# Kernel optimization log

Measured on AMD Instinct MI355X. Metric: run time of the kernel, lower is better.

The kernel has to match this reference:

```python
import jax, jax.numpy as jnp
import numpy as np

EPS = 1e-8            # EpisodicMemory.eps
TEMPERATURE = 0.25    # default temperature in query()


def setup_inputs() -> dict:
    key = jax.random.key(0)
    k1, k2, k3 = jax.random.split(key, 3)
    B, N, KD, VD, TOPK = 512, 500000, 128, 64, 16
    queries = jax.random.normal(k1, (B, KD), dtype=jnp.float32)
    # stored keys are L2-normalized at insert time
    keys = jax.random.normal(k2, (N, KD), dtype=jnp.float32)
    keys = keys / jnp.clip(jnp.linalg.norm(keys, axis=1, keepdims=True), EPS, None)
    values = jax.random.normal(k3, (N, VD), dtype=jnp.float32)
    return {"queries": queries, "keys": keys, "values": values, "topk": TOPK}


def reference(queries, keys, values, topk):
    # cosine similarity: normalize queries (keys already normalized in memory)
    qn = queries / jnp.clip(jnp.linalg.norm(queries, axis=1, keepdims=True), EPS, None)
    scores = (qn @ keys.T) / max(1e-6, TEMPERATURE)          # [B, N]
    topv, topidx = jax.lax.top_k(scores, topk)               # [B, K], [B, K]
    # stable exp-softmax with eps in the denominator (as in torch source)
    topv_exp = jnp.exp(topv - jnp.max(topv, axis=1, keepdims=True))
    topw = topv_exp / (jnp.sum(topv_exp, axis=1, keepdims=True) + EPS)
    vals = values[topidx]                                    # gather: [B, K, VD]
    retrieved = jnp.einsum('bk,bkd->bd', topw, vals)         # [B, VD]
    return retrieved, topw, topidx
```

## Files before the change

### kernel.cpp

```cpp
#include <hip/hip_runtime.h>
#include <hip/hip_bf16.h>

#define NB 512
#define KD 128
#define VD 64
#define NKEYS 500000
#define TOPK 16
#define CH 1024
#define NCHUNK 489
#define NCAND (NCHUNK*4)

typedef __attribute__((ext_vector_type(8))) short bf8s;
typedef __attribute__((ext_vector_type(4))) float f4;

__device__ __forceinline__ unsigned f2bf(float x) {
  union { float f; unsigned u; } v; v.f = x;
  return (v.u + 0x7fffu + ((v.u >> 16) & 1u)) >> 16;
}

__global__ __launch_bounds__(128) void qnorm_kernel(const float* __restrict__ q,
                                                    float* __restrict__ qn_f,
                                                    short* __restrict__ qn_bf) {
  int b = blockIdx.x, t = threadIdx.x;
  float x = q[b*KD + t];
  float s = x * x;
  #pragma unroll
  for (int o = 32; o > 0; o >>= 1) s += __shfl_down(s, o);
  __shared__ float p[2];
  if ((t & 63) == 0) p[t >> 6] = s;
  __syncthreads();
  float norm = sqrtf(p[0] + p[1]);
  norm = fmaxf(norm, 1e-8f);
  float v = x * (4.0f / norm);
  qn_f[b*KD + t] = v;
  qn_bf[b*KD + t] = (short)f2bf(v);
}

__global__ __launch_bounds__(256) void score_filter_kernel(
    const float* __restrict__ keys, const short* __restrict__ qn_bf,
    float* __restrict__ cand_val, int* __restrict__ cand_idx) {
  __shared__ float slds[256 * 17];
  const int chunk = blockIdx.x, gy = blockIdx.y;
  const int tid  = threadIdx.x;
  const int wave = tid >> 6, lane = tid & 63;
  const int col  = lane & 15, quad = lane >> 4;

  bf8s afrag[4][4];
  const int qbase = gy*256 + wave*64;
  #pragma unroll
  for (int mt = 0; mt < 4; mt++)
    #pragma unroll
    for (int ks = 0; ks < 4; ks++)
      afrag[mt][ks] = *(const bf8s*)(qn_bf + (qbase + mt*16 + col)*KD + ks*32 + quad*8);

  float tv0=-1e30f, tv1=-1e30f, tv2=-1e30f, tv3=-1e30f;
  int   ti0=0, ti1=0, ti2=0, ti3=0;
  const int nchunk0 = chunk * CH;

  for (int nt = 0; nt < CH/16; nt++) {
    const int nb = nchunk0 + nt*16;
    int r = nb + col; if (r > NKEYS-1) r = NKEYS-1;
    const float* kp = keys + (size_t)r*KD + quad*8;
    bf8s bfrag[4];
    #pragma unroll
    for (int ks = 0; ks < 4; ks++) {
      f4 x0 = *(const f4*)(kp + ks*32);
      f4 x1 = *(const f4*)(kp + ks*32 + 4);
      bf8s tt;
      tt[0]=(short)f2bf(x0[0]); tt[1]=(short)f2bf(x0[1]);
      tt[2]=(short)f2bf(x0[2]); tt[3]=(short)f2bf(x0[3]);
      tt[4]=(short)f2bf(x1[0]); tt[5]=(short)f2bf(x1[1]);
      tt[6]=(short)f2bf(x1[2]); tt[7]=(short)f2bf(x1[3]);
      bfrag[ks] = tt;
    }
    f4 acc[4];
    #pragma unroll
    for (int mt = 0; mt < 4; mt++) { acc[mt][0]=0.f; acc[mt][1]=0.f; acc[mt][2]=0.f; acc[mt][3]=0.f; }
    #pragma unroll
    for (int ks = 0; ks < 4; ks++)
      #pragma unroll
      for (int mt = 0; mt < 4; mt++)
        acc[mt] = __builtin_amdgcn_mfma_f32_16x16x32_bf16(afrag[mt][ks], bfrag[ks], acc[mt], 0, 0, 0);
    #pragma unroll
    for (int mt = 0; mt < 4; mt++)
      #pragma unroll
      for (int rg = 0; rg < 4; rg++)
        slds[(wave*64 + mt*16 + quad*4 + rg)*17 + col] = acc[mt][rg];
    __syncthreads();
    #pragma unroll
    for (int c = 0; c < 16; c++) {
      int n = nb + c;
      float v = slds[tid*17 + c];
      if (v > tv3 && n < NKEYS) {
        if (v > tv0)      { tv3=tv2;ti3=ti2; tv2=tv1;ti2=ti1; tv1=tv0;ti1=ti0; tv0=v;ti0=n; }
        else if (v > tv1) { tv3=tv2;ti3=ti2; tv2=tv1;ti2=ti1; tv1=v;ti1=n; }
        else if (v > tv2) { tv3=tv2;ti3=ti2; tv2=v;ti2=n; }
        else              { tv3=v;ti3=n; }
      }
    }
    __syncthreads();
  }
  const int gq = gy*256 + tid;
  const size_t o = ((size_t)gq*NCHUNK + chunk)*4;
  cand_val[o+0]=tv0; cand_val[o+1]=tv1; cand_val[o+2]=tv2; cand_val[o+3]=tv3;
  cand_idx[o+0]=ti0; cand_idx[o+1]=ti1; cand_idx[o+2]=ti2; cand_idx[o+3]=ti3;
}

__global__ __launch_bounds__(256) void merge_rescore_kernel(
    const float* __restrict__ qn_f, const float* __restrict__ keys,
    const float* __restrict__ values, const float* __restrict__ cand_val,
    const int* __restrict__ cand_idx, float* __restrict__ out) {
  const int b = blockIdx.x, t = threadIdx.x;
  const int lane = t & 63, wave = t >> 6;
  __shared__ float cv[NCAND]; __shared__ int ci[NCAND];
  __shared__ float qs[KD];
  __shared__ float redv[4]; __shared__ int redp[4];
  __shared__ float rv[32];  __shared__ int ri[32];
  __shared__ float sval[16]; __shared__ int sidx[16]; __shared__ float sw[16];

  if (t < KD) qs[t] = qn_f[b*KD + t];
  for (int i = t; i < NCAND; i += 256) {
    cv[i] = cand_val[(size_t)b*NCAND + i];
    ci[i] = cand_idx[(size_t)b*NCAND + i];
  }
  __syncthreads();

  for (int rdx = 0; rdx < 32; rdx++) {
    float mv = -1e30f; int mp = 0;
    for (int i = t; i < NCAND; i += 256) { float v = cv[i]; if (v > mv) { mv = v; mp = i; } }
    #pragma unroll
    for (int o = 32; o > 0; o >>= 1) {
      float ov = __shfl_down(mv, o); int op = __shfl_down(mp, o);
      if (ov > mv) { mv = ov; mp = op; }
    }
    if (lane == 0) { redv[wave] = mv; redp[wave] = mp; }
    __syncthreads();
    if (t == 0) {
      float bv = redv[0]; int bp = redp[0];
      for (int w = 1; w < 4; w++) if (redv[w] > bv) { bv = redv[w]; bp = redp[w]; }
      ri[rdx] = ci[bp];
      cv[bp] = -1e30f;
    }
    __syncthreads();
  }

  {
    int c = t >> 3, dg = t & 7;
    int n = ri[c];
    const float* kr = keys + (size_t)n*KD + dg*16;
    float part = 0.f;
    #pragma unroll
    for (int j = 0; j < 16; j++) part += kr[j] * qs[dg*16 + j];
    #pragma unroll
    for (int o = 4; o > 0; o >>= 1) part += __shfl_down(part, o, 8);
    if (dg == 0) rv[c] = part;
  }
  __syncthreads();

  if (t < 32) {
    float v = rv[t]; int idx = ri[t];
    int rank = 0;
    for (int j = 0; j < 32; j++) {
      float vj = rv[j]; int ij = ri[j];
      rank += (vj > v) || (vj == v && ij < idx);
    }
    if (rank < TOPK) { sval[rank] = v; sidx[rank] = idx; }
  }
  __syncthreads();

  if (t < TOPK) {
    float m = sval[0];
    float e = expf(sval[t] - m);
    float s = e;
    #pragma unroll
    for (int o = 8; o > 0; o >>= 1) s += __shfl_down(s, o, 16);
    s = __shfl(s, 0, 16);
    float w = e / (s + 1e-8f);
    sw[t] = w;
    out[NB*VD + b*TOPK + t] = w;
    out[NB*VD + NB*TOPK + b*TOPK + t] = (float)sidx[t];
  }
  __syncthreads();

  if (t < VD) {
    float acc = 0.f;
    #pragma unroll
    for (int k = 0; k < TOPK; k++) acc += sw[k] * values[(size_t)sidx[k]*VD + t];
    out[b*VD + t] = acc;
  }
}

extern "C" void kernel_launch(void* const* d_in, const int* in_sizes, int n_in,
                              void* d_out, int out_size, void* d_ws, size_t ws_size,
                              hipStream_t stream) {
  const float* queries = (const float*)d_in[0];
  const float* keys    = (const float*)d_in[1];
  const float* values  = (const float*)d_in[2];
  float* out = (float*)d_out;

  char* ws = (char*)d_ws;
  float* qn_f  = (float*)ws;
  short* qn_bf = (short*)(ws + (size_t)NB*KD*4);
  float* cand_val = (float*)(ws + (size_t)NB*KD*4 + (size_t)NB*KD*2);
  int*   cand_idx = (int*)((char*)cand_val + (size_t)NB*NCHUNK*4*sizeof(float));

  qnorm_kernel<<<NB, KD, 0, stream>>>(queries, qn_f, qn_bf);
  score_filter_kernel<<<dim3(NCHUNK, 2), 256, 0, stream>>>(keys, qn_bf, cand_val, cand_idx);
  merge_rescore_kernel<<<NB, 256, 0, stream>>>(qn_f, keys, values, cand_val, cand_idx, out);
}
```

Baseline: 659.2 us.

## Radix-select candidate merge and prefetch key rows in score kernel

The merge kernel replaces 32 rounds of block-wide argmax over ~2000 candidates with a radix histogram select on the float bits. The select keeps up to 64 survivors at or above the threshold and rescores them in fp32 before ranking to top-16. The score kernel software-prefetches the next 16 key rows into registers during current compute and uses raw barriers that wait only on LDS. This cuts the serial barrier-heavy selection and hides global load latency, at the cost of more registers and a larger rescoring set.

```diff
diff --git a/kernel.cpp b/kernel.cpp
--- a/kernel.cpp
+++ b/kernel.cpp
@@ -9,6 +9,7 @@
 #define CH 1024
 #define NCHUNK 489
 #define NCAND (NCHUNK*4)
+#define CBUF 64
 
 typedef __attribute__((ext_vector_type(8))) short bf8s;
 typedef __attribute__((ext_vector_type(4))) float f4;
@@ -16,6 +17,11 @@
 __device__ __forceinline__ unsigned f2bf(float x) {
   union { float f; unsigned u; } v; v.f = x;
   return (v.u + 0x7fffu + ((v.u >> 16) & 1u)) >> 16;
+}
+
+__device__ __forceinline__ void barrier_lgkm() {
+  asm volatile("s_waitcnt lgkmcnt(0)" ::: "memory");
+  __builtin_amdgcn_s_barrier();
 }
 
 __global__ __launch_bounds__(128) void qnorm_kernel(const float* __restrict__ q,
@@ -57,21 +63,37 @@
   int   ti0=0, ti1=0, ti2=0, ti3=0;
   const int nchunk0 = chunk * CH;
 
+  f4 x0[4], x1[4];
+  {
+    int r = nchunk0 + col; if (r > NKEYS-1) r = NKEYS-1;
+    const float* kp = keys + (size_t)r*KD + quad*8;
+    #pragma unroll
+    for (int ks = 0; ks < 4; ks++) {
+      x0[ks] = *(const f4*)(kp + ks*32);
+      x1[ks] = *(const f4*)(kp + ks*32 + 4);
+    }
+  }
+
   for (int nt = 0; nt < CH/16; nt++) {
     const int nb = nchunk0 + nt*16;
-    int r = nb + col; if (r > NKEYS-1) r = NKEYS-1;
-    const float* kp = keys + (size_t)r*KD + quad*8;
     bf8s bfrag[4];
     #pragma unroll
     for (int ks = 0; ks < 4; ks++) {
-      f4 x0 = *(const f4*)(kp + ks*32);
-      f4 x1 = *(const f4*)(kp + ks*32 + 4);
       bf8s tt;
-      tt[0]=(short)f2bf(x0[0]); tt[1]=(short)f2bf(x0[1]);
-      tt[2]=(short)f2bf(x0[2]); tt[3]=(short)f2bf(x0[3]);
-      tt[4]=(short)f2bf(x1[0]); tt[5]=(short)f2bf(x1[1]);
-      tt[6]=(short)f2bf(x1[2]); tt[7]=(short)f2bf(x1[3]);
+      tt[0]=(short)f2bf(x0[ks][0]); tt[1]=(short)f2bf(x0[ks][1]);
+      tt[2]=(short)f2bf(x0[ks][2]); tt[3]=(short)f2bf(x0[ks][3]);
+      tt[4]=(short)f2bf(x1[ks][0]); tt[5]=(short)f2bf(x1[ks][1]);
+      tt[6]=(short)f2bf(x1[ks][2]); tt[7]=(short)f2bf(x1[ks][3]);
       bfrag[ks] = tt;
+    }
+    if (nt + 1 < CH/16) {
+      int r = nb + 16 + col; if (r > NKEYS-1) r = NKEYS-1;
+      const float* kp = keys + (size_t)r*KD + quad*8;
+      #pragma unroll
+      for (int ks = 0; ks < 4; ks++) {
+        x0[ks] = *(const f4*)(kp + ks*32);
+        x1[ks] = *(const f4*)(kp + ks*32 + 4);
+      }
     }
     f4 acc[4];
     #pragma unroll
@@ -86,7 +108,7 @@
       #pragma unroll
       for (int rg = 0; rg < 4; rg++)
         slds[(wave*64 + mt*16 + quad*4 + rg)*17 + col] = acc[mt][rg];
-    __syncthreads();
+    barrier_lgkm();
     #pragma unroll
     for (int c = 0; c < 16; c++) {
       int n = nb + c;
@@ -98,7 +120,7 @@
         else              { tv3=v;ti3=n; }
       }
     }
-    __syncthreads();
+    barrier_lgkm();
   }
   const int gq = gy*256 + tid;
   const size_t o = ((size_t)gq*NCHUNK + chunk)*4;
@@ -112,55 +134,93 @@
     const int* __restrict__ cand_idx, float* __restrict__ out) {
   const int b = blockIdx.x, t = threadIdx.x;
   const int lane = t & 63, wave = t >> 6;
-  __shared__ float cv[NCAND]; __shared__ int ci[NCAND];
   __shared__ float qs[KD];
-  __shared__ float redv[4]; __shared__ int redp[4];
-  __shared__ float rv[32];  __shared__ int ri[32];
-  __shared__ float sval[16]; __shared__ int sidx[16]; __shared__ float sw[16];
+  __shared__ unsigned hist[256];
+  __shared__ int wtot[4];
+  __shared__ int s_bound, s_above, s_bcnt, s_cnt;
+  __shared__ float rv[CBUF]; __shared__ int ri[CBUF];
+  __shared__ float sval[TOPK]; __shared__ int sidx[TOPK]; __shared__ float sw[TOPK];
 
   if (t < KD) qs[t] = qn_f[b*KD + t];
-  for (int i = t; i < NCAND; i += 256) {
-    cv[i] = cand_val[(size_t)b*NCAND + i];
-    ci[i] = cand_idx[(size_t)b*NCAND + i];
-  }
-  __syncthreads();
-
-  for (int rdx = 0; rdx < 32; rdx++) {
-    float mv = -1e30f; int mp = 0;
-    for (int i = t; i < NCAND; i += 256) { float v = cv[i]; if (v > mv) { mv = v; mp = i; } }
-    #pragma unroll
-    for (int o = 32; o > 0; o >>= 1) {
-      float ov = __shfl_down(mv, o); int op = __shfl_down(mp, o);
-      if (ov > mv) { mv = ov; mp = op; }
-    }
-    if (lane == 0) { redv[wave] = mv; redp[wave] = mp; }
-    __syncthreads();
-    if (t == 0) {
-      float bv = redv[0]; int bp = redp[0];
-      for (int w = 1; w < 4; w++) if (redv[w] > bv) { bv = redv[w]; bp = redp[w]; }
-      ri[rdx] = ci[bp];
-      cv[bp] = -1e30f;
-    }
-    __syncthreads();
-  }
+
+  unsigned u[8]; int id[8];
+  #pragma unroll
+  for (int j = 0; j < 8; j++) {
+    int i = t + j*256;
+    if (i < NCAND) {
+      union { float f; unsigned q; } cvt; cvt.f = cand_val[(size_t)b*NCAND + i];
+      unsigned m = cvt.q;
+      m = (m & 0x80000000u) ? ~m : (m | 0x80000000u);
+      u[j] = m; id[j] = cand_idx[(size_t)b*NCAND + i];
+    } else { u[j] = 0u; id[j] = -1; }
+  }
+
+  unsigned prefix = 0; int above = 0; unsigned thr = 0; bool done = false;
+  #pragma unroll 1
+  for (int pass = 0; pass < 3 && !done; pass++) {
+    const int shift = 24 - 8*pass;
+    hist[t] = 0u;
+    __syncthreads();
+    #pragma unroll
+    for (int j = 0; j < 8; j++) {
+      bool ok = (pass == 0) || ((u[j] >> (shift + 8)) == prefix);
+      if (ok) atomicAdd(&hist[(u[j] >> shift) & 255u], 1u);
+    }
+    __syncthreads();
+    int h = (int)hist[t];
+    int s = h;
+    #pragma unroll
+    for (int o = 1; o < 64; o <<= 1) {
+      int nv = __shfl_down(s, o);
+      if (lane + o < 64) s += nv;
+    }
+    if (lane == 0) wtot[wave] = s;
+    __syncthreads();
+    int add = 0;
+    for (int g = wave + 1; g < 4; g++) add += wtot[g];
+    int S = s + add;
+    if (above + S >= 32 && above + S - h < 32) {
+      s_bound = t; s_above = above + S - h; s_bcnt = h;
+    }
+    __syncthreads();
+    prefix = (prefix << 8) | (unsigned)s_bound;
+    above  = s_above;
+    if (s_above + s_bcnt <= CBUF || pass == 2) { thr = prefix << shift; done = true; }
+    __syncthreads();
+  }
+
+  if (t == 0) s_cnt = 0;
+  __syncthreads();
+  #pragma unroll
+  for (int j = 0; j < 8; j++) {
+    if (id[j] >= 0 && u[j] >= thr) {
+      int p = atomicAdd(&s_cnt, 1);
+      if (p < CBUF) ri[p] = id[j];
+    }
+  }
+  __syncthreads();
+  const int C = min(s_cnt, CBUF);
+  if (t >= C && t < CBUF) ri[t] = 0x7fffffff;
+  __syncthreads();
 
   {
-    int c = t >> 3, dg = t & 7;
-    int n = ri[c];
-    const float* kr = keys + (size_t)n*KD + dg*16;
+    int c = t >> 2, dg = t & 3;
     float part = 0.f;
-    #pragma unroll
-    for (int j = 0; j < 16; j++) part += kr[j] * qs[dg*16 + j];
-    #pragma unroll
-    for (int o = 4; o > 0; o >>= 1) part += __shfl_down(part, o, 8);
-    if (dg == 0) rv[c] = part;
-  }
-  __syncthreads();
-
-  if (t < 32) {
+    if (c < C) {
+      const float* kr = keys + (size_t)ri[c]*KD + dg*32;
+      #pragma unroll
+      for (int j = 0; j < 32; j++) part += kr[j] * qs[dg*32 + j];
+    }
+    part += __shfl_down(part, 2, 4);
+    part += __shfl_down(part, 1, 4);
+    if (dg == 0) rv[c] = (c < C) ? part : -1e30f;
+  }
+  __syncthreads();
+
+  if (t < CBUF) {
     float v = rv[t]; int idx = ri[t];
     int rank = 0;
-    for (int j = 0; j < 32; j++) {
+    for (int j = 0; j < CBUF; j++) {
       float vj = rv[j]; int ij = ri[j];
       rank += (vj > v) || (vj == v && ij < idx);
     }
@@ -171,11 +231,11 @@
   if (t < TOPK) {
     float m = sval[0];
     float e = expf(sval[t] - m);
-    float s = e;
-    #pragma unroll
-    for (int o = 8; o > 0; o >>= 1) s += __shfl_down(s, o, 16);
-    s = __shfl(s, 0, 16);
-    float w = e / (s + 1e-8f);
+    float s2 = e;
+    #pragma unroll
+    for (int o = 8; o > 0; o >>= 1) s2 += __shfl_down(s2, o, 16);
+    s2 = __shfl(s2, 0, 16);
+    float w = e / (s2 + 1e-8f);
     sw[t] = w;
     out[NB*VD + b*TOPK + t] = w;
     out[NB*VD + NB*TOPK + b*TOPK + t] = (float)sidx[t];
```

Measured after the change: 638.1 us. -3.2%, faster.
